# Kernel tuning notes

Measured on AMD Instinct MI355X. Metric: run time of the kernel, lower is better.

Reference implementation:

```python
import jax, jax.numpy as jnp
import numpy as np

B = 4096      # batch
NS = 40       # number of single-valued features (length=1)
NM = 8        # number of multi-valued features
L = 8         # length of each multi-valued feature
V = 10000     # vocab per feature (table rows = V+1, row 0 = padding)
D = 64        # per-feature embedding dim (get_emb_dim(10000,64) == 64)
T = 16        # num_ns_tokens
DM = 512      # d_model
TOTAL = (NS + NM) * D      # 3072, total_emb_dim (pad = 0)
CHUNK = TOTAL // T         # 192, chunk_dim
LN_EPS = 1e-5


def setup_inputs() -> dict:
    key = jax.random.key(0)
    ks = jax.random.split(key, 10)
    int_feats = jax.random.randint(ks[0], (B, NS + NM * L), 0, V + 1)
    emb_single = jax.random.normal(ks[1], (NS, V + 1, D), jnp.float32) * 0.02
    emb_multi = jax.random.normal(ks[2], (NM, V + 1, D), jnp.float32) * 0.02
    h = TOTAL // 4
    lhuc_w1 = jax.random.normal(ks[3], (TOTAL, h), jnp.float32) * 0.02
    lhuc_b1 = jnp.zeros((h,), jnp.float32)
    lhuc_w2 = jax.random.normal(ks[4], (h, TOTAL), jnp.float32) * 0.02
    lhuc_b2 = jnp.zeros((TOTAL,), jnp.float32)
    proj_w = jax.random.normal(ks[5], (T, CHUNK, DM), jnp.float32) * 0.05
    proj_b = jnp.zeros((T, DM), jnp.float32)
    ln_g = jnp.ones((T, DM), jnp.float32)
    ln_b = jnp.zeros((T, DM), jnp.float32)
    return {
        "int_feats": int_feats,
        "emb_single": emb_single, "emb_multi": emb_multi,
        "lhuc_w1": lhuc_w1, "lhuc_b1": lhuc_b1,
        "lhuc_w2": lhuc_w2, "lhuc_b2": lhuc_b2,
        "proj_w": proj_w, "proj_b": proj_b, "ln_g": ln_g, "ln_b": ln_b,
    }


def reference(int_feats, emb_single, emb_multi, lhuc_w1, lhuc_b1,
              lhuc_w2, lhuc_b2, proj_w, proj_b, ln_g, ln_b):
    b = int_feats.shape[0]
    # --- single-valued features: per-feature gather (padding_idx=0 -> zero) ---
    idx_s = int_feats[:, :NS]                                   # (B, NS)
    es = emb_single[jnp.arange(NS)[None, :], idx_s]             # (B, NS, D)
    es = es * (idx_s != 0)[..., None].astype(es.dtype)
    # --- multi-valued features: gather + masked mean pool ---
    idx_m = int_feats[:, NS:].reshape(b, NM, L)                 # (B, NM, L)
    em = emb_multi[jnp.arange(NM)[None, :, None], idx_m]        # (B, NM, L, D)
    mask = (idx_m != 0)[..., None].astype(em.dtype)             # (B, NM, L, 1)
    denom = jnp.maximum(mask.sum(axis=2), 1.0)                  # (B, NM, 1)
    pooled = (em * mask).sum(axis=2) / denom                    # (B, NM, D)
    # --- concat (group order == feature order) ---
    cat = jnp.concatenate([es.reshape(b, NS * D), pooled.reshape(b, NM * D)], axis=-1)  # (B, TOTAL)
    # --- LHUC gating MLP ---
    h = jax.nn.silu(cat @ lhuc_w1 + lhuc_b1)
    gate = jax.nn.sigmoid(h @ lhuc_w2 + lhuc_b2)
    x = (cat * gate * 2.0).reshape(b, T, CHUNK)                 # pad == 0
    # --- per-token Linear + LayerNorm (batched over tokens) ---
    y = jnp.einsum('btc,tcd->btd', x, proj_w) + proj_b          # (B, T, DM)
    mu = y.mean(axis=-1, keepdims=True)
    var = ((y - mu) ** 2).mean(axis=-1, keepdims=True)
    y = (y - mu) * jax.lax.rsqrt(var + LN_EPS) * ln_g + ln_b
    return y
```

## Files before the change

kernel.cpp:

```cpp
#include <hip/hip_runtime.h>
#include <hip/hip_bf16.h>


typedef unsigned short u16;
typedef unsigned int u32;
typedef __attribute__((ext_vector_type(8))) short s16x8;
typedef __attribute__((ext_vector_type(4))) float f32x4;

#define NSF 40
#define NMF 8
#define LLEN 8
#define VROWS 10001
#define DD 64
#define TT 16
#define DMOD 512
#define TOTAL 3072
#define CHUNKC 192
#define NFEAT 104

__device__ __forceinline__ u16 f2bf(float f) {
  __hip_bfloat16 h = __float2bfloat16(f);
  return *reinterpret_cast<u16*>(&h);
}
__device__ __forceinline__ float bf2f(u16 u) {
  __hip_bfloat16 h;
  *reinterpret_cast<u16*>(&h) = u;
  return __bfloat162float(h);
}

__device__ __forceinline__ void gll16(const u16* g, u16* l) {
  __builtin_amdgcn_global_load_lds((const __attribute__((address_space(1))) void*)g,
                                   (__attribute__((address_space(3))) void*)l, 16, 0, 0);
}

__global__ void transpose_all_kernel(const float* __restrict__ w1, u16* __restrict__ w1t,
                                     const float* __restrict__ w2, u16* __restrict__ w2t,
                                     const float* __restrict__ pw, u16* __restrict__ pwt) {
  __shared__ float tile[32][33];
  int id = blockIdx.x;
  const float* src; u16* dst; int R, C, bx, by;
  if (id < 2304)      { src = w1; dst = w1t; R = 3072; C = 768;  bx = id % 24; by = id / 24; }
  else if (id < 4608) { int l = id - 2304; src = w2; dst = w2t; R = 768; C = 3072; bx = l % 96; by = l / 96; }
  else                { int l = id - 4608; int t = l / 96; int r2 = l % 96;
                        src = pw + (long)t * CHUNKC * DMOD; dst = pwt + (long)t * DMOD * CHUNKC;
                        R = CHUNKC; C = DMOD; bx = r2 % 16; by = r2 / 16; }
  int c0 = bx * 32, r0 = by * 32;
#pragma unroll
  for (int i = 0; i < 32; i += 8)
    tile[threadIdx.y + i][threadIdx.x] = src[(long)(r0 + threadIdx.y + i) * C + c0 + threadIdx.x];
  __syncthreads();
#pragma unroll
  for (int i = 0; i < 32; i += 8)
    dst[(long)(c0 + threadIdx.y + i) * R + r0 + threadIdx.x] = f2bf(tile[threadIdx.x][threadIdx.y + i]);
}

__global__ __launch_bounds__(256) void embed_kernel(const int* __restrict__ feats,
                                                    const float* __restrict__ tabS,
                                                    const float* __restrict__ tabM,
                                                    u16* __restrict__ catb) {
  int b = blockIdx.x;
  int tid = threadIdx.x;
  int d4 = tid & 15;
  int g = tid >> 4;
  const int* fr = feats + (long)b * NFEAT;
  u16* crow = catb + (long)b * TOTAL;

  for (int f = g; f < NSF; f += 16) {
    int idx = fr[f];
    float4 v = make_float4(0.f, 0.f, 0.f, 0.f);
    if (idx) v = *reinterpret_cast<const float4*>(tabS + ((long)f * VROWS + idx) * DD + d4 * 4);
    ushort4 pk = {f2bf(v.x), f2bf(v.y), f2bf(v.z), f2bf(v.w)};
    *reinterpret_cast<ushort4*>(crow + f * DD + d4 * 4) = pk;
  }
  int m = g >> 1, half = g & 1;
  float sx = 0.f, sy = 0.f, sz = 0.f, sw = 0.f, cnt = 0.f;
#pragma unroll
  for (int l = 0; l < 4; l++) {
    int idx = fr[NSF + m * LLEN + half * 4 + l];
    if (idx) {
      float4 e = *reinterpret_cast<const float4*>(tabM + ((long)m * VROWS + idx) * DD + d4 * 4);
      sx += e.x; sy += e.y; sz += e.z; sw += e.w; cnt += 1.f;
    }
  }
  sx += __shfl_xor(sx, 16, 64);
  sy += __shfl_xor(sy, 16, 64);
  sz += __shfl_xor(sz, 16, 64);
  sw += __shfl_xor(sw, 16, 64);
  cnt += __shfl_xor(cnt, 16, 64);
  if (!half) {
    float inv = 1.f / fmaxf(cnt, 1.f);
    ushort4 pk = {f2bf(sx * inv), f2bf(sy * inv), f2bf(sz * inv), f2bf(sw * inv)};
    *reinterpret_cast<ushort4*>(crow + NSF * DD + m * DD + d4 * 4) = pk;
  }
}

template <int N, int K, int BM, int BN, int EPI>
__global__ __launch_bounds__(256) void gemm_kernel(const u16* __restrict__ A,
                                                   const u16* __restrict__ Bt,
                                                   const float* __restrict__ bias,
                                                   const u16* __restrict__ aux,
                                                   u16* __restrict__ Out) {
  constexpr int WCOL = (BN >= 128) ? 2 : 1;
  constexpr int WROW = 4 / WCOL;
  constexpr int MF = (BM / WROW) / 16;
  constexpr int NF = (BN / WCOL) / 16;
  constexpr int NT = K / 32;

  __shared__ u16 lA[2][BM * 32];
  __shared__ u16 lB[2][BN * 32];

  const int tid = threadIdx.x;
  const int w = tid >> 6;
  const int lane = tid & 63;
  const int l15 = lane & 15, hi = lane >> 4;
  const int wr = w / WCOL, wc = w % WCOL;

  const int nblk = gridDim.x * gridDim.y;
  const int lid = blockIdx.x + gridDim.x * blockIdx.y;
  const int sw = (lid & 7) * (nblk >> 3) + (lid >> 3);
  const int m0 = (sw / gridDim.x) * BM, n0 = (sw % gridDim.x) * BN;

  f32x4 acc[MF][NF];
#pragma unroll
  for (int m = 0; m < MF; m++)
#pragma unroll
    for (int n = 0; n < NF; n++) acc[m][n] = (f32x4){0.f, 0.f, 0.f, 0.f};

  const int srow = tid >> 2;
  const int sc8 = (tid & 3) * 8;

  auto stage = [&](int buf, int t) {
    const u16* Ab = A + (long)m0 * K + t * 32;
    const u16* Bb = Bt + (long)n0 * K + t * 32;
#pragma unroll
    for (int i = 0; i < BM / 64; i++)
      gll16(Ab + (long)(i * 64 + srow) * K + sc8, &lA[buf][(i * 256 + w * 64) * 8]);
#pragma unroll
    for (int i = 0; i < BN / 64; i++)
      gll16(Bb + (long)(i * 64 + srow) * K + sc8, &lB[buf][(i * 256 + w * 64) * 8]);
  };

  stage(0, 0);
  __syncthreads();

#pragma unroll 2
  for (int t = 0; t < NT; t++) {
    int buf = t & 1;
    if (t + 1 < NT) stage(buf ^ 1, t + 1);
    s16x8 af[MF], bf[NF];
#pragma unroll
    for (int m = 0; m < MF; m++)
      af[m] = *reinterpret_cast<const s16x8*>(&lA[buf][(wr * (MF * 16) + m * 16 + l15) * 32 + hi * 8]);
#pragma unroll
    for (int n = 0; n < NF; n++)
      bf[n] = *reinterpret_cast<const s16x8*>(&lB[buf][(wc * (NF * 16) + n * 16 + l15) * 32 + hi * 8]);
#pragma unroll
    for (int m = 0; m < MF; m++)
#pragma unroll
      for (int n = 0; n < NF; n++)
        acc[m][n] = __builtin_amdgcn_mfma_f32_16x16x32_bf16(af[m], bf[n], acc[m][n], 0, 0, 0);
    __syncthreads();
  }

#pragma unroll
  for (int n = 0; n < NF; n++) {
    int col = n0 + wc * (NF * 16) + n * 16 + l15;
    float bs = bias[col];
#pragma unroll
    for (int m = 0; m < MF; m++) {
      int rbase = m0 + wr * (MF * 16) + m * 16 + hi * 4;
#pragma unroll
      for (int j = 0; j < 4; j++) {
        int row = rbase + j;
        float z = acc[m][n][j] + bs;
        float o;
        if (EPI == 0) {
          o = z / (1.f + __expf(-z));
        } else {
          float gs = 1.f / (1.f + __expf(-z));
          float xv = bf2f(aux[(long)row * N + col]);
          o = xv * gs * 2.f;
        }
        Out[(long)row * N + col] = f2bf(o);
      }
    }
  }
}

__global__ __launch_bounds__(512) void proj_ln_kernel(const u16* __restrict__ xb,
                                                      const u16* __restrict__ pwt,
                                                      const float* __restrict__ pb,
                                                      const float* __restrict__ lng,
                                                      const float* __restrict__ lnb,
                                                      float* __restrict__ out) {
  __shared__ u16 lA[2][64 * 32];
  __shared__ u16 lB[2][512 * 32];
  __shared__ float sred[64][4][2];

  const int tid = threadIdx.x;
  const int w = tid >> 6, lane = tid & 63;
  const int l15 = lane & 15, hi = lane >> 4;
  const int wr = w >> 2, wc = w & 3;

  const int lid = blockIdx.x + gridDim.x * blockIdx.y;
  const int sw = (lid & 7) * ((gridDim.x * gridDim.y) >> 3) + (lid >> 3);
  const int t = sw / gridDim.x;
  const int m0 = (sw % gridDim.x) * 64;

  const u16* Ab = xb + (long)m0 * TOTAL + t * CHUNKC;
  const u16* Bb = pwt + (long)t * DMOD * CHUNKC;

  const int srow = tid >> 2;
  const int sc8 = (tid & 3) * 8;

  auto stage = [&](int buf, int kt) {
    if (w < 4)
      gll16(Ab + (long)srow * TOTAL + kt * 32 + sc8, &lA[buf][w * 512]);
#pragma unroll
    for (int i = 0; i < 4; i++)
      gll16(Bb + (long)(i * 128 + srow) * CHUNKC + kt * 32 + sc8,
            &lB[buf][i * 4096 + w * 512]);
  };

  f32x4 acc[2][8];
#pragma unroll
  for (int m = 0; m < 2; m++)
#pragma unroll
    for (int n = 0; n < 8; n++) acc[m][n] = (f32x4){0.f, 0.f, 0.f, 0.f};

  stage(0, 0);
  __syncthreads();

#pragma unroll
  for (int kt = 0; kt < 6; kt++) {
    int buf = kt & 1;
    if (kt + 1 < 6) stage(buf ^ 1, kt + 1);
    s16x8 af[2], bfr[8];
#pragma unroll
    for (int m = 0; m < 2; m++)
      af[m] = *reinterpret_cast<const s16x8*>(&lA[buf][(wr * 32 + m * 16 + l15) * 32 + hi * 8]);
#pragma unroll
    for (int n = 0; n < 8; n++)
      bfr[n] = *reinterpret_cast<const s16x8*>(&lB[buf][(wc * 128 + n * 16 + l15) * 32 + hi * 8]);
#pragma unroll
    for (int m = 0; m < 2; m++)
#pragma unroll
      for (int n = 0; n < 8; n++)
        acc[m][n] = __builtin_amdgcn_mfma_f32_16x16x32_bf16(af[m], bfr[n], acc[m][n], 0, 0, 0);
    __syncthreads();
  }

  float sum[2][4], sq[2][4];
#pragma unroll
  for (int m = 0; m < 2; m++)
#pragma unroll
    for (int j = 0; j < 4; j++) { sum[m][j] = 0.f; sq[m][j] = 0.f; }

#pragma unroll
  for (int n = 0; n < 8; n++) {
    float bs = pb[t * DMOD + wc * 128 + n * 16 + l15];
#pragma unroll
    for (int m = 0; m < 2; m++)
#pragma unroll
      for (int j = 0; j < 4; j++) {
        float v = acc[m][n][j] + bs;
        acc[m][n][j] = v;
        sum[m][j] += v;
        sq[m][j] += v * v;
      }
  }
#pragma unroll
  for (int m = 0; m < 2; m++)
#pragma unroll
    for (int j = 0; j < 4; j++) {
#pragma unroll
      for (int o = 1; o < 16; o <<= 1) {
        sum[m][j] += __shfl_xor(sum[m][j], o, 64);
        sq[m][j] += __shfl_xor(sq[m][j], o, 64);
      }
    }
  if (l15 == 0) {
#pragma unroll
    for (int m = 0; m < 2; m++)
#pragma unroll
      for (int j = 0; j < 4; j++) {
        int r = wr * 32 + m * 16 + hi * 4 + j;
        sred[r][wc][0] = sum[m][j];
        sred[r][wc][1] = sq[m][j];
      }
  }
  __syncthreads();

  float mean[2][4], rstd[2][4];
#pragma unroll
  for (int m = 0; m < 2; m++)
#pragma unroll
    for (int j = 0; j < 4; j++) {
      int r = wr * 32 + m * 16 + hi * 4 + j;
      float s = sred[r][0][0] + sred[r][1][0] + sred[r][2][0] + sred[r][3][0];
      float q = sred[r][0][1] + sred[r][1][1] + sred[r][2][1] + sred[r][3][1];
      float mu = s * (1.f / 512.f);
      float var = q * (1.f / 512.f) - mu * mu;
      mean[m][j] = mu;
      rstd[m][j] = rsqrtf(var + 1e-5f);
    }
#pragma unroll
  for (int n = 0; n < 8; n++) {
    int c = wc * 128 + n * 16 + l15;
    float g = lng[t * DMOD + c], bb = lnb[t * DMOD + c];
#pragma unroll
    for (int m = 0; m < 2; m++)
#pragma unroll
      for (int j = 0; j < 4; j++) {
        int r = wr * 32 + m * 16 + hi * 4 + j;
        float o = (acc[m][n][j] - mean[m][j]) * rstd[m][j] * g + bb;
        out[((long)(m0 + r) * TT + t) * DMOD + c] = o;
      }
  }
}

extern "C" void kernel_launch(void* const* d_in, const int* in_sizes, int n_in,
                              void* d_out, int out_size, void* d_ws, size_t ws_size,
                              hipStream_t stream) {
  const int* feats = (const int*)d_in[0];
  const float* embS = (const float*)d_in[1];
  const float* embM = (const float*)d_in[2];
  const float* w1 = (const float*)d_in[3];
  const float* b1 = (const float*)d_in[4];
  const float* w2 = (const float*)d_in[5];
  const float* b2 = (const float*)d_in[6];
  const float* pw = (const float*)d_in[7];
  const float* pb = (const float*)d_in[8];
  const float* lng = (const float*)d_in[9];
  const float* lnb = (const float*)d_in[10];
  float* out = (float*)d_out;

  char* p = (char*)d_ws;
  u16* catb = (u16*)p; p += (size_t)4096 * 3072 * 2;
  u16* hb   = (u16*)p; p += (size_t)4096 * 768 * 2;
  u16* xb   = (u16*)p; p += (size_t)4096 * 3072 * 2;
  u16* w1t  = (u16*)p; p += (size_t)768 * 3072 * 2;
  u16* w2t  = (u16*)p; p += (size_t)3072 * 768 * 2;
  u16* pwt  = (u16*)p; p += (size_t)16 * 512 * 192 * 2;

  transpose_all_kernel<<<6144, dim3(32, 8), 0, stream>>>(w1, w1t, w2, w2t, pw, pwt);

  embed_kernel<<<4096, 256, 0, stream>>>(feats, embS, embM, catb);

  gemm_kernel<768, 3072, 128, 128, 0><<<dim3(768 / 128, 4096 / 128), 256, 0, stream>>>(
      catb, w1t, b1, nullptr, hb);

  gemm_kernel<3072, 768, 128, 128, 1><<<dim3(3072 / 128, 4096 / 128), 256, 0, stream>>>(
      hb, w2t, b2, catb, xb);

  proj_ln_kernel<<<dim3(4096 / 64, 16), 512, 0, stream>>>(xb, pwt, pb, lng, lnb, out);
}
```

Baseline: 433.0 us.

## Parameterize GEMM K-tile and use smaller tiles for first LHUC GEMM

Adds a BK template parameter so the GEMM stages wider K slices per iteration and issues several MFMA k-steps per barrier. The first LHUC GEMM (N=768, K=3072) switches to 64x64 tiles with BK=64, raising its block count from 192 to 768 so more CUs have work. The block-index swizzle is removed from both the GEMM and the projection+LayerNorm kernels in favor of plain blockIdx mapping. Smaller tiles mean less operand reuse per block, and dropping the swizzle may change L2 locality.

```diff
diff --git a/kernel.cpp b/kernel.cpp
--- a/kernel.cpp
+++ b/kernel.cpp
@@ -94,7 +94,7 @@
   }
 }
 
-template <int N, int K, int BM, int BN, int EPI>
+template <int N, int K, int BM, int BN, int BK, int EPI>
 __global__ __launch_bounds__(256) void gemm_kernel(const u16* __restrict__ A,
                                                    const u16* __restrict__ Bt,
                                                    const float* __restrict__ bias,
@@ -104,21 +104,19 @@
   constexpr int WROW = 4 / WCOL;
   constexpr int MF = (BM / WROW) / 16;
   constexpr int NF = (BN / WCOL) / 16;
-  constexpr int NT = K / 32;
-
-  __shared__ u16 lA[2][BM * 32];
-  __shared__ u16 lB[2][BN * 32];
+  constexpr int NT = K / BK;
+  constexpr int KS = BK / 32;
+  constexpr int RPP = 2048 / BK;
+
+  __shared__ u16 lA[2][BM * BK];
+  __shared__ u16 lB[2][BN * BK];
 
   const int tid = threadIdx.x;
   const int w = tid >> 6;
   const int lane = tid & 63;
   const int l15 = lane & 15, hi = lane >> 4;
   const int wr = w / WCOL, wc = w % WCOL;
-
-  const int nblk = gridDim.x * gridDim.y;
-  const int lid = blockIdx.x + gridDim.x * blockIdx.y;
-  const int sw = (lid & 7) * (nblk >> 3) + (lid >> 3);
-  const int m0 = (sw / gridDim.x) * BM, n0 = (sw % gridDim.x) * BN;
+  const int m0 = blockIdx.y * BM, n0 = blockIdx.x * BN;
 
   f32x4 acc[MF][NF];
 #pragma unroll
@@ -126,18 +124,18 @@
 #pragma unroll
     for (int n = 0; n < NF; n++) acc[m][n] = (f32x4){0.f, 0.f, 0.f, 0.f};
 
-  const int srow = tid >> 2;
-  const int sc8 = (tid & 3) * 8;
+  const int srow = tid / (BK / 8);
+  const int sc8 = (tid % (BK / 8)) * 8;
 
   auto stage = [&](int buf, int t) {
-    const u16* Ab = A + (long)m0 * K + t * 32;
-    const u16* Bb = Bt + (long)n0 * K + t * 32;
-#pragma unroll
-    for (int i = 0; i < BM / 64; i++)
-      gll16(Ab + (long)(i * 64 + srow) * K + sc8, &lA[buf][(i * 256 + w * 64) * 8]);
-#pragma unroll
-    for (int i = 0; i < BN / 64; i++)
-      gll16(Bb + (long)(i * 64 + srow) * K + sc8, &lB[buf][(i * 256 + w * 64) * 8]);
+    const u16* Ab = A + (long)m0 * K + t * BK;
+    const u16* Bb = Bt + (long)n0 * K + t * BK;
+#pragma unroll
+    for (int i = 0; i < BM / RPP; i++)
+      gll16(Ab + (long)(i * RPP + srow) * K + sc8, &lA[buf][i * 2048 + w * 512]);
+#pragma unroll
+    for (int i = 0; i < BN / RPP; i++)
+      gll16(Bb + (long)(i * RPP + srow) * K + sc8, &lB[buf][i * 2048 + w * 512]);
   };
 
   stage(0, 0);
@@ -147,18 +145,26 @@
   for (int t = 0; t < NT; t++) {
     int buf = t & 1;
     if (t + 1 < NT) stage(buf ^ 1, t + 1);
-    s16x8 af[MF], bf[NF];
+    s16x8 af[MF][KS], bf[NF][KS];
 #pragma unroll
     for (int m = 0; m < MF; m++)
-      af[m] = *reinterpret_cast<const s16x8*>(&lA[buf][(wr * (MF * 16) + m * 16 + l15) * 32 + hi * 8]);
+#pragma unroll
+      for (int ks = 0; ks < KS; ks++)
+        af[m][ks] = *reinterpret_cast<const s16x8*>(
+            &lA[buf][(wr * (MF * 16) + m * 16 + l15) * BK + ks * 32 + hi * 8]);
 #pragma unroll
     for (int n = 0; n < NF; n++)
-      bf[n] = *reinterpret_cast<const s16x8*>(&lB[buf][(wc * (NF * 16) + n * 16 + l15) * 32 + hi * 8]);
-#pragma unroll
-    for (int m = 0; m < MF; m++)
-#pragma unroll
-      for (int n = 0; n < NF; n++)
-        acc[m][n] = __builtin_amdgcn_mfma_f32_16x16x32_bf16(af[m], bf[n], acc[m][n], 0, 0, 0);
+#pragma unroll
+      for (int ks = 0; ks < KS; ks++)
+        bf[n][ks] = *reinterpret_cast<const s16x8*>(
+            &lB[buf][(wc * (NF * 16) + n * 16 + l15) * BK + ks * 32 + hi * 8]);
+#pragma unroll
+    for (int ks = 0; ks < KS; ks++)
+#pragma unroll
+      for (int m = 0; m < MF; m++)
+#pragma unroll
+        for (int n = 0; n < NF; n++)
+          acc[m][n] = __builtin_amdgcn_mfma_f32_16x16x32_bf16(af[m][ks], bf[n][ks], acc[m][n], 0, 0, 0);
     __syncthreads();
   }
 
@@ -197,15 +203,12 @@
   __shared__ u16 lB[2][512 * 32];
   __shared__ float sred[64][4][2];
 
+  const int t = blockIdx.y;
+  const int m0 = blockIdx.x * 64;
   const int tid = threadIdx.x;
   const int w = tid >> 6, lane = tid & 63;
   const int l15 = lane & 15, hi = lane >> 4;
   const int wr = w >> 2, wc = w & 3;
-
-  const int lid = blockIdx.x + gridDim.x * blockIdx.y;
-  const int sw = (lid & 7) * ((gridDim.x * gridDim.y) >> 3) + (lid >> 3);
-  const int t = sw / gridDim.x;
-  const int m0 = (sw % gridDim.x) * 64;
 
   const u16* Ab = xb + (long)m0 * TOTAL + t * CHUNKC;
   const u16* Bb = pwt + (long)t * DMOD * CHUNKC;
@@ -347,10 +350,10 @@
 
   embed_kernel<<<4096, 256, 0, stream>>>(feats, embS, embM, catb);
 
-  gemm_kernel<768, 3072, 128, 128, 0><<<dim3(768 / 128, 4096 / 128), 256, 0, stream>>>(
+  gemm_kernel<768, 3072, 64, 64, 64, 0><<<dim3(768 / 64, 4096 / 64), 256, 0, stream>>>(
       catb, w1t, b1, nullptr, hb);
 
-  gemm_kernel<3072, 768, 128, 128, 1><<<dim3(3072 / 128, 4096 / 128), 256, 0, stream>>>(
+  gemm_kernel<3072, 768, 128, 128, 32, 1><<<dim3(3072 / 128, 4096 / 128), 256, 0, stream>>>(
       hb, w2t, b2, catb, xb);
 
   proj_ln_kernel<<<dim3(4096 / 64, 16), 512, 0, stream>>>(xb, pwt, pb, lng, lnb, out);
```

Result: faster. 412.0 us (-4.9%).
